# Performance work log

Hardware: AMD Instinct MI355X
Metric: run time of the kernel (lower is better)

## Reference

```python
import jax, jax.numpy as jnp
import numpy as np

N, E, F_IN, GCH, H, HID, NOUT, NG = 5000, 15000, 300, 2048, 4, 2048, 768, 128
NEG_SLOPE = 0.2


def gat_conv(x, W, att_src, att_dst, bias, src, dst):
    # x: [N, Fin]; W: [Fin, H*C]; att_*: [H, C]; bias: [H*C]
    n = x.shape[0]
    h = (x @ W).reshape(n, H, GCH)                      # [N,H,C]
    a_src = (h * att_src).sum(-1)                       # [N,H]
    a_dst = (h * att_dst).sum(-1)                       # [N,H]
    e = jax.nn.leaky_relu(a_src[src] + a_dst[dst], NEG_SLOPE)  # [E,H]
    m = jax.ops.segment_max(e, dst, num_segments=n)     # segment softmax over dst
    e = jnp.exp(e - m[dst])
    s = jax.ops.segment_sum(e, dst, num_segments=n)
    alpha = e / (s[dst] + 1e-16)                        # [E,H]
    msg = h[src] * alpha[:, :, None]                    # [E,H,C]
    out = jax.ops.segment_sum(msg, dst, num_segments=n) # [N,H,C]
    return out.reshape(n, H * GCH) + bias


def setup_inputs() -> dict:
    key = jax.random.key(0)
    ks = jax.random.split(key, 32)
    d = {}
    d['x'] = jax.random.normal(ks[0], (N, F_IN), jnp.float32)
    d['edge_index'] = jax.random.randint(ks[1], (2, E), 0, N, jnp.int32)
    d['batch'] = jnp.sort(jax.random.randint(ks[2], (N,), 0, NG, jnp.int32))
    dims_in = [F_IN, HID, HID]
    i = 3
    for l, fin in enumerate(dims_in, 1):
        sc = 1.0 / np.sqrt(fin)
        d[f'W{l}'] = jax.random.normal(ks[i], (fin, H * GCH), jnp.float32) * sc; i += 1
        d[f'asrc{l}'] = jax.random.normal(ks[i], (H, GCH), jnp.float32) * 0.02; i += 1
        d[f'adst{l}'] = jax.random.normal(ks[i], (H, GCH), jnp.float32) * 0.02; i += 1
        d[f'bc{l}'] = jnp.zeros((H * GCH,), jnp.float32)
        d[f'Wh{l}'] = jax.random.normal(ks[i], (H * GCH, HID), jnp.float32) * (1.0 / np.sqrt(H * GCH)); i += 1
        d[f'bh{l}'] = jnp.zeros((HID,), jnp.float32)
    d['Wm1'] = jax.random.normal(ks[i], (GCH, 2048), jnp.float32) * (1.0 / np.sqrt(GCH)); i += 1
    d['bm1'] = jnp.zeros((2048,), jnp.float32)
    d['Wm2'] = jax.random.normal(ks[i], (2048, NOUT), jnp.float32) * (1.0 / np.sqrt(2048)); i += 1
    d['bm2'] = jnp.zeros((NOUT,), jnp.float32)
    d['ln_g'] = jnp.ones((NOUT,), jnp.float32)
    d['ln_b'] = jnp.zeros((NOUT,), jnp.float32)
    return d


def reference(x, edge_index, batch,
              W1, asrc1, adst1, bc1, Wh1, bh1,
              W2, asrc2, adst2, bc2, Wh2, bh2,
              W3, asrc3, adst3, bc3, Wh3, bh3,
              Wm1, bm1, Wm2, bm2, ln_g, ln_b):
    n = x.shape[0]
    # PyG GATConv adds self-loops by default
    loops = jnp.arange(n, dtype=edge_index.dtype)
    src = jnp.concatenate([edge_index[0], loops])
    dst = jnp.concatenate([edge_index[1], loops])

    h = gat_conv(x, W1, asrc1, adst1, bc1, src, dst)
    h = jax.nn.relu(h @ Wh1 + bh1)
    h = gat_conv(h, W2, asrc2, adst2, bc2, src, dst)
    h = jax.nn.relu(h @ Wh2 + bh2)
    h = gat_conv(h, W3, asrc3, adst3, bc3, src, dst)
    h = h @ Wh3 + bh3                                   # no relu after head_linear3

    # global mean pool over graphs
    sums = jax.ops.segment_sum(h, batch, num_segments=NG)
    cnt = jax.ops.segment_sum(jnp.ones((n,), h.dtype), batch, num_segments=NG)
    g = sums / jnp.maximum(cnt, 1.0)[:, None]           # [NG, 2048]

    g = jax.nn.relu(g @ Wm1 + bm1)
    g = g @ Wm2 + bm2                                   # [NG, NOUT]
    mu = g.mean(-1, keepdims=True)
    var = ((g - mu) ** 2).mean(-1, keepdims=True)
    return (g - mu) / jnp.sqrt(var + 1e-5) * ln_g + ln_b
```

## Files before the change

### kernel.cpp

```cpp
#include <hip/hip_runtime.h>

typedef unsigned short u16;
typedef __attribute__((ext_vector_type(8))) short short8;
typedef __attribute__((ext_vector_type(4))) float f32x4;

__device__ inline u16 f2bf(float f){
  unsigned int u = __builtin_bit_cast(unsigned int, f);
  u += 0x7fffu + ((u >> 16) & 1u);
  return (u16)(u >> 16);
}
__device__ inline float bf2f(u16 h){
  unsigned int u = ((unsigned int)h) << 16;
  return __builtin_bit_cast(float, u);
}

typedef __attribute__((address_space(1))) const void* as1_t;
typedef __attribute__((address_space(3))) void* as3_t;
__device__ __forceinline__ void gload16(const u16* g, u16* l) {
  __builtin_amdgcn_global_load_lds((as1_t)g, (as3_t)l, 16, 0, 0);
}

#define BARRIER() asm volatile("s_barrier" ::: "memory")
#define VMCNT4()  asm volatile("s_waitcnt vmcnt(4)" ::: "memory")
#define VMCNT0()  asm volatile("s_waitcnt vmcnt(0)" ::: "memory")
#define LGKM0()   asm volatile("s_waitcnt lgkmcnt(0)" ::: "memory")

__global__ __launch_bounds__(256) void transpose_cast(
    const float* __restrict__ W, u16* __restrict__ Wt, int K, int N, int Kpad)
{
  __shared__ float tile[32][33];
  int k0 = blockIdx.x * 32, n0 = blockIdx.y * 32;
  int tx = threadIdx.x & 31, ty = threadIdx.x >> 5;
#pragma unroll
  for (int i = 0; i < 4; ++i) {
    int k = k0 + ty + i * 8;
    float v = 0.f;
    if (k < K && (n0 + tx) < N) v = W[(size_t)k * N + n0 + tx];
    tile[ty + i * 8][tx] = v;
  }
  __syncthreads();
#pragma unroll
  for (int i = 0; i < 4; ++i) {
    int nn = n0 + ty + i * 8;
    if (nn < N) Wt[(size_t)nn * Kpad + k0 + tx] = f2bf(tile[tx][ty + i * 8]);
  }
}

__global__ void cast_pad(const float* __restrict__ x, u16* __restrict__ xb,
                         int R, int C, int Cp)
{
  int i = blockIdx.x * 256 + threadIdx.x;
  if (i >= R * Cp) return;
  int r = i / Cp, c = i % Cp;
  xb[i] = f2bf(c < C ? x[(size_t)r * C + c] : 0.f);
}

__global__ __launch_bounds__(256) void wvec(
    const float* __restrict__ W, const float* __restrict__ asrc,
    const float* __restrict__ adst, float* __restrict__ wsd, int Fp)
{
  int f = blockIdx.x;
  int w = threadIdx.x >> 6, lane = threadIdx.x & 63;
  const float* wr = W + (size_t)f * 8192 + w * 2048;
  const float* as = asrc + w * 2048;
  const float* ad = adst + w * 2048;
  float ss = 0.f, dd = 0.f;
#pragma unroll
  for (int i = 0; i < 8; ++i) {
    int c = lane * 4 + i * 256;
    f32x4 wv = *reinterpret_cast<const f32x4*>(wr + c);
    f32x4 av = *reinterpret_cast<const f32x4*>(as + c);
    f32x4 dv = *reinterpret_cast<const f32x4*>(ad + c);
#pragma unroll
    for (int j = 0; j < 4; ++j) { ss += wv[j] * av[j]; dd += wv[j] * dv[j]; }
  }
  for (int off = 32; off; off >>= 1) {
    ss += __shfl_down(ss, off);
    dd += __shfl_down(dd, off);
  }
  if (lane == 0) { wsd[w * Fp + f] = ss; wsd[(4 + w) * Fp + f] = dd; }
}

__global__ __launch_bounds__(256) void a_score(
    const u16* __restrict__ xb, const float* __restrict__ wsd,
    float* __restrict__ a_s, float* __restrict__ a_d, int Fp)
{
  int n = blockIdx.x, tid = threadIdx.x, lane = tid & 63, w = tid >> 6;
  float s[4] = {0.f,0.f,0.f,0.f}, d[4] = {0.f,0.f,0.f,0.f};
  int f = tid * 8;
  if (f < Fp) {
    short8 v = *reinterpret_cast<const short8*>(xb + (size_t)n * Fp + f);
#pragma unroll
    for (int j = 0; j < 8; ++j) {
      float xv = bf2f((u16)v[j]);
#pragma unroll
      for (int h = 0; h < 4; ++h) {
        s[h] += xv * wsd[h * Fp + f + j];
        d[h] += xv * wsd[(4 + h) * Fp + f + j];
      }
    }
  }
  __shared__ float red[4][8];
#pragma unroll
  for (int h = 0; h < 4; ++h) {
    for (int off = 32; off; off >>= 1) {
      s[h] += __shfl_down(s[h], off);
      d[h] += __shfl_down(d[h], off);
    }
  }
  if (lane == 0) {
#pragma unroll
    for (int h = 0; h < 4; ++h) { red[w][h] = s[h]; red[w][4 + h] = d[h]; }
  }
  __syncthreads();
  if (tid < 8) {
    float t = red[0][tid] + red[1][tid] + red[2][tid] + red[3][tid];
    if (tid < 4) a_s[n * 4 + tid] = t;
    else         a_d[n * 4 + tid - 4] = t;
  }
}

__global__ __launch_bounds__(256) void bias_fold(
    const float* __restrict__ bc, const float* __restrict__ Wh,
    const float* __restrict__ bh, float* __restrict__ bhp)
{
  int b = blockIdx.x;
  int oc = threadIdx.x & 31, ks = threadIdx.x >> 5;
  int o = b * 32 + oc;
  float acc = 0.f;
  for (int k = ks * 1024; k < ks * 1024 + 1024; ++k)
    acc += bc[k] * Wh[(size_t)k * 2048 + o];
  __shared__ float red[8][33];
  red[ks][oc] = acc;
  __syncthreads();
  if (threadIdx.x < 32) {
    float t = 0.f;
#pragma unroll
    for (int i = 0; i < 8; ++i) t += red[i][threadIdx.x];
    bhp[b * 32 + threadIdx.x] = t + bh[b * 32 + threadIdx.x];
  }
}

__global__ __launch_bounds__(512, 2) void gemm8p(
    const u16* __restrict__ A, const u16* __restrict__ B, u16* __restrict__ C,
    int M, int N, int K, int lda, int ldb, int ldc, int headed)
{
  __shared__ alignas(16) u16 lds[65536];
  int tid = threadIdx.x, wave = tid >> 6, lane = tid & 63;
  int wm = wave >> 2, wn = wave & 3;
  int tile_m = blockIdx.y * 256, tile_n = blockIdx.x * 256;
  int NT = K >> 6;
  int hoff = headed ? ((tile_m >> 11) << 11) : 0;
  int abase = headed ? (tile_m & 2047) : tile_m;

  const u16* sA[2]; const u16* sB[2];
  int dq[2];
#pragma unroll
  for (int q = 0; q < 2; ++q) {
    int row = q * 128 + (tid >> 2);
    int cg  = (tid & 3) ^ ((row >> 1) & 3);
    sA[q] = A + (size_t)(abase + row) * lda + hoff + cg * 8;
    sB[q] = B + (size_t)(tile_n + row) * ldb + hoff + cg * 8;
    dq[q] = q * 4096 + tid * 8;
  }

  int l15 = lane & 15, c4 = lane >> 4;
  int aoff[8], boff[4];
#pragma unroll
  for (int mi = 0; mi < 8; ++mi) {
    int r = wm * 128 + mi * 16 + l15;
    aoff[mi] = r * 32 + ((c4 ^ ((r >> 1) & 3)) * 8);
  }
#pragma unroll
  for (int ni = 0; ni < 4; ++ni) {
    int r = wn * 64 + ni * 16 + l15;
    boff[ni] = r * 32 + ((c4 ^ ((r >> 1) & 3)) * 8);
  }

  f32x4 acc[8][4];
#pragma unroll
  for (int mi = 0; mi < 8; ++mi)
#pragma unroll
    for (int ni = 0; ni < 4; ++ni) { f32x4 z = {0.f,0.f,0.f,0.f}; acc[mi][ni] = z; }

#define DSRA(fa, mb, base) \
  fa[0] = *reinterpret_cast<const short8*>(&lds[(base) + aoff[(mb)+0]]); \
  fa[1] = *reinterpret_cast<const short8*>(&lds[(base) + aoff[(mb)+1]]); \
  fa[2] = *reinterpret_cast<const short8*>(&lds[(base) + aoff[(mb)+2]]); \
  fa[3] = *reinterpret_cast<const short8*>(&lds[(base) + aoff[(mb)+3]]);
#define DSRB(fb, base) \
  fb[0] = *reinterpret_cast<const short8*>(&lds[(base) + boff[0]]); \
  fb[1] = *reinterpret_cast<const short8*>(&lds[(base) + boff[1]]); \
  fb[2] = *reinterpret_cast<const short8*>(&lds[(base) + boff[2]]); \
  fb[3] = *reinterpret_cast<const short8*>(&lds[(base) + boff[3]]);
#define MM16(mb, fa, fb) \
  _Pragma("unroll") for (int mi = 0; mi < 4; ++mi) \
  _Pragma("unroll") for (int ni = 0; ni < 4; ++ni) \
    acc[(mb)+mi][ni] = __builtin_amdgcn_mfma_f32_16x16x32_bf16(fa[mi], fb[ni], acc[(mb)+mi][ni], 0, 0, 0);
#define PH_SYNC() BARRIER(); LGKM0(); __builtin_amdgcn_sched_barrier(0)
#define PRIO1() __builtin_amdgcn_s_setprio(1)
#define PRIO0() __builtin_amdgcn_s_setprio(0)

#pragma unroll
  for (int q = 0; q < 2; ++q) {
    gload16(sA[q],      &lds[0     + dq[q]]);
    gload16(sB[q],      &lds[16384 + dq[q]]);
    gload16(sA[q] + 32, &lds[8192  + dq[q]]);
    gload16(sB[q] + 32, &lds[24576 + dq[q]]);
  }
  VMCNT0();
  BARRIER();

  for (int t = 0; t < NT; ++t) {
    int cb = (t & 1) * 32768;
    int nb = cb ^ 32768;
    bool st = (t + 1) < NT;
    int ke = (t + 1) * 64;
    short8 fa[4], fb0[4], fb1[4];
    DSRA(fa, 0, cb + 0);
    DSRB(fb0, cb + 16384);
    if (st) { gload16(sA[0] + ke, &lds[nb + dq[0]]);
              gload16(sA[1] + ke, &lds[nb + dq[1]]); }
    PH_SYNC(); PRIO1(); MM16(0, fa, fb0); PRIO0();
    BARRIER();
    DSRA(fa, 4, cb + 0);
    if (st) { gload16(sB[0] + ke, &lds[nb + 16384 + dq[0]]);
              gload16(sB[1] + ke, &lds[nb + 16384 + dq[1]]); }
    PH_SYNC(); PRIO1(); MM16(4, fa, fb0); PRIO0();
    if (st) { VMCNT4(); } else { VMCNT0(); }
    BARRIER();
    DSRA(fa, 0, cb + 8192);
    DSRB(fb1, cb + 24576);
    if (st) { gload16(sA[0] + ke + 32, &lds[nb + 8192 + dq[0]]);
              gload16(sA[1] + ke + 32, &lds[nb + 8192 + dq[1]]); }
    PH_SYNC(); PRIO1(); MM16(0, fa, fb1); PRIO0();
    BARRIER();
    DSRA(fa, 4, cb + 8192);
    if (st) { gload16(sB[0] + ke + 32, &lds[nb + 24576 + dq[0]]);
              gload16(sB[1] + ke + 32, &lds[nb + 24576 + dq[1]]); }
    PH_SYNC(); PRIO1(); MM16(4, fa, fb1); PRIO0();
    if (st) { VMCNT4(); }
    BARRIER();
  }

  int rq = (lane >> 4) * 4;
#pragma unroll
  for (int mi = 0; mi < 8; ++mi)
#pragma unroll
    for (int ni = 0; ni < 4; ++ni) {
      int col = tile_n + wn * 64 + ni * 16 + l15;
#pragma unroll
      for (int j = 0; j < 4; ++j) {
        int row = tile_m + wm * 128 + mi * 16 + rq + j;
        if (row < M) C[(size_t)row * ldc + col] = f2bf(acc[mi][ni][j]);
      }
    }
#undef DSRA
#undef DSRB
#undef MM16
#undef PH_SYNC
#undef PRIO1
#undef PRIO0
}

__global__ __launch_bounds__(256) void gemm_bt(
    const u16* __restrict__ A, const u16* __restrict__ B,
    float* __restrict__ Cf, u16* __restrict__ Cb,
    const float* __restrict__ bias, int M, int N, int K, int relu)
{
  __shared__ alignas(16) u16 As[128 * 32];
  __shared__ alignas(16) u16 Bs[128 * 32];
  int tid = threadIdx.x;
  int wave = tid >> 6, lane = tid & 63;
  int wr = wave >> 1, wc = wave & 1;
  int tile_m = blockIdx.y * 128, tile_n = blockIdx.x * 128;

  int sr = wave * 16 + (lane >> 2);
  int sc = (lane & 3) * 8;
  const u16* gA0 = A + (size_t)(tile_m + sr) * K + sc;
  const u16* gA1 = A + (size_t)(tile_m + 64 + sr) * K + sc;
  const u16* gB0 = B + (size_t)(tile_n + sr) * K + sc;
  const u16* gB1 = B + (size_t)(tile_n + 64 + sr) * K + sc;
  u16* lA0 = &As[wave * 512];
  u16* lA1 = &As[2048 + wave * 512];
  u16* lB0 = &Bs[wave * 512];
  u16* lB1 = &Bs[2048 + wave * 512];

  f32x4 acc[4][4];
#pragma unroll
  for (int mi = 0; mi < 4; ++mi)
#pragma unroll
    for (int ni = 0; ni < 4; ++ni) { f32x4 z = {0.f,0.f,0.f,0.f}; acc[mi][ni] = z; }

  int lrow = lane & 15, lk = (lane >> 4) * 8;

  for (int k0 = 0; k0 < K; k0 += 32) {
    gload16(gA0 + k0, lA0);
    gload16(gA1 + k0, lA1);
    gload16(gB0 + k0, lB0);
    gload16(gB1 + k0, lB1);
    __syncthreads();
    short8 af[4], bfr[4];
#pragma unroll
    for (int mi = 0; mi < 4; ++mi)
      af[mi] = *reinterpret_cast<const short8*>(&As[(wr * 64 + mi * 16 + lrow) * 32 + lk]);
#pragma unroll
    for (int ni = 0; ni < 4; ++ni)
      bfr[ni] = *reinterpret_cast<const short8*>(&Bs[(wc * 64 + ni * 16 + lrow) * 32 + lk]);
#pragma unroll
    for (int mi = 0; mi < 4; ++mi)
#pragma unroll
      for (int ni = 0; ni < 4; ++ni)
        acc[mi][ni] = __builtin_amdgcn_mfma_f32_16x16x32_bf16(af[mi], bfr[ni], acc[mi][ni], 0, 0, 0);
    __syncthreads();
  }

  int rquad = (lane >> 4) * 4;
#pragma unroll
  for (int mi = 0; mi < 4; ++mi)
#pragma unroll
    for (int ni = 0; ni < 4; ++ni) {
      int col = tile_n + wc * 64 + ni * 16 + lrow;
      float bv = bias ? bias[col] : 0.f;
#pragma unroll
      for (int j = 0; j < 4; ++j) {
        int row = tile_m + wr * 64 + mi * 16 + rquad + j;
        if (row < M) {
          float v = acc[mi][ni][j] + bv;
          if (relu) v = fmaxf(v, 0.f);
          if (Cb) Cb[(size_t)row * N + col] = f2bf(v);
          else    Cf[(size_t)row * N + col] = v;
        }
      }
    }
}

__global__ void zero_int(int* p, int n){ int i = blockIdx.x*256+threadIdx.x; if (i < n) p[i] = 0; }

__global__ void count_deg(const int* __restrict__ ei, int E, int Nn, int* __restrict__ deg){
  int e = blockIdx.x*256+threadIdx.x; if (e >= E + Nn) return;
  int d = (e < E) ? ei[E + e] : (e - E);
  atomicAdd(&deg[d], 1);
}

__global__ void scan_deg(const int* __restrict__ deg, int* __restrict__ row_st,
                         int* __restrict__ cursor, int Nn){
  __shared__ int partial[256];
  int tid = threadIdx.x;
  int chunk = (Nn + 255) / 256;
  int start = tid * chunk;
  int sum = 0;
  for (int i = 0; i < chunk; ++i) { int idx = start + i; if (idx < Nn) sum += deg[idx]; }
  partial[tid] = sum;
  __syncthreads();
  if (tid == 0) { int acc = 0; for (int i = 0; i < 256; ++i) { int t = partial[i]; partial[i] = acc; acc += t; } }
  __syncthreads();
  int acc = partial[tid];
  for (int i = 0; i < chunk; ++i) {
    int idx = start + i;
    if (idx < Nn) { row_st[idx] = acc; cursor[idx] = acc; acc += deg[idx]; }
  }
  if (tid == 255) row_st[Nn] = acc;
}

__global__ void scatter_edges(const int* __restrict__ ei, int E, int Nn,
                              int* __restrict__ cursor, int* __restrict__ srcs){
  int e = blockIdx.x*256+threadIdx.x; if (e >= E + Nn) return;
  int s = (e < E) ? ei[e]     : (e - E);
  int d = (e < E) ? ei[E + e] : (e - E);
  int pos = atomicAdd(&cursor[d], 1);
  srcs[pos] = s;
}

__global__ void edge_softmax(const int* __restrict__ row_st, const int* __restrict__ srcs,
                             const float* __restrict__ a_s, const float* __restrict__ a_d,
                             float* __restrict__ alpha, int Nn){
  int t = blockIdx.x*256+threadIdx.x;
  if (t >= Nn * 4) return;
  int n = t >> 2, hh = t & 3;
  int b = row_st[n], e = row_st[n + 1];
  float ad = a_d[n * 4 + hh];
  float m = -1e30f;
  for (int p = b; p < e; ++p) {
    float x = a_s[srcs[p] * 4 + hh] + ad;
    x = x > 0.f ? x : 0.2f * x;
    alpha[p * 4 + hh] = x;
    m = fmaxf(m, x);
  }
  float ssum = 0.f;
  for (int p = b; p < e; ++p) {
    float ex = expf(alpha[p * 4 + hh] - m);
    alpha[p * 4 + hh] = ex;
    ssum += ex;
  }
  float inv = 1.f / (ssum + 1e-16f);
  for (int p = b; p < e; ++p) alpha[p * 4 + hh] *= inv;
}

__global__ __launch_bounds__(256) void aggregate2(
    const u16* __restrict__ z, const float* __restrict__ alpha,
    const int* __restrict__ row_st, const int* __restrict__ srcs,
    const float* __restrict__ bhp, u16* __restrict__ out, int relu)
{
  int n = blockIdx.x, tid = threadIdx.x;
  int c = tid * 8;
  float acc[8];
#pragma unroll
  for (int q = 0; q < 8; ++q) acc[q] = 0.f;
  int b = row_st[n], e = row_st[n + 1];
  for (int p = b; p < e; ++p) {
    int s = srcs[p];
    const u16* zr = z + (size_t)s * 8192 + c;
    float a0 = alpha[p * 4 + 0], a1 = alpha[p * 4 + 1];
    float a2 = alpha[p * 4 + 2], a3 = alpha[p * 4 + 3];
    short8 v0 = *reinterpret_cast<const short8*>(zr);
    short8 v1 = *reinterpret_cast<const short8*>(zr + 2048);
    short8 v2 = *reinterpret_cast<const short8*>(zr + 4096);
    short8 v3 = *reinterpret_cast<const short8*>(zr + 6144);
#pragma unroll
    for (int q = 0; q < 8; ++q)
      acc[q] += a0 * bf2f((u16)v0[q]) + a1 * bf2f((u16)v1[q])
              + a2 * bf2f((u16)v2[q]) + a3 * bf2f((u16)v3[q]);
  }
  short8 ov;
#pragma unroll
  for (int q = 0; q < 8; ++q) {
    float v = acc[q] + bhp[c + q];
    if (relu) v = fmaxf(v, 0.f);
    ov[q] = (short)f2bf(v);
  }
  *reinterpret_cast<short8*>(out + (size_t)n * 2048 + c) = ov;
}

__global__ __launch_bounds__(256) void pool_mean(
    const u16* __restrict__ hf, const int* __restrict__ batch,
    u16* __restrict__ g, int Nn)
{
  int gid = blockIdx.x, tid = threadIdx.x;
  int s1, s2;
  { int l = 0, h = Nn; while (l < h) { int m = (l + h) >> 1; if (batch[m] < gid) l = m + 1; else h = m; } s1 = l; }
  { int l = 0, h = Nn; while (l < h) { int m = (l + h) >> 1; if (batch[m] < gid + 1) l = m + 1; else h = m; } s2 = l; }
  float inv = 1.f / fmaxf((float)(s2 - s1), 1.f);
  float acc[8];
#pragma unroll
  for (int q = 0; q < 8; ++q) acc[q] = 0.f;
  for (int r = s1; r < s2; ++r) {
    short8 v = *reinterpret_cast<const short8*>(hf + (size_t)r * 2048 + tid * 8);
#pragma unroll
    for (int q = 0; q < 8; ++q) acc[q] += bf2f((u16)v[q]);
  }
  short8 ov;
#pragma unroll
  for (int q = 0; q < 8; ++q) ov[q] = (short)f2bf(acc[q] * inv);
  *reinterpret_cast<short8*>(g + (size_t)gid * 2048 + tid * 8) = ov;
}

__global__ __launch_bounds__(256) void layernorm_768(
    const float* __restrict__ x, const float* __restrict__ gam,
    const float* __restrict__ bet, float* __restrict__ out)
{
  int row = blockIdx.x, tid = threadIdx.x, lane = tid & 63, w = tid >> 6;
  __shared__ float sh[8];
  float v0 = x[row * 768 + tid];
  float v1 = x[row * 768 + 256 + tid];
  float v2 = x[row * 768 + 512 + tid];
  float s = v0 + v1 + v2;
  for (int off = 32; off; off >>= 1) s += __shfl_down(s, off);
  if (lane == 0) sh[w] = s;
  __syncthreads();
  if (tid == 0) sh[4] = (sh[0] + sh[1] + sh[2] + sh[3]) / 768.f;
  __syncthreads();
  float mu = sh[4];
  float d0 = v0 - mu, d1 = v1 - mu, d2 = v2 - mu;
  float q = d0 * d0 + d1 * d1 + d2 * d2;
  for (int off = 32; off; off >>= 1) q += __shfl_down(q, off);
  if (lane == 0) sh[w] = q;
  __syncthreads();
  if (tid == 0) sh[5] = rsqrtf((sh[0] + sh[1] + sh[2] + sh[3]) / 768.f + 1e-5f);
  __syncthreads();
  float rstd = sh[5];
  out[row * 768 + tid]       = d0 * rstd * gam[tid]       + bet[tid];
  out[row * 768 + 256 + tid] = d1 * rstd * gam[256 + tid] + bet[256 + tid];
  out[row * 768 + 512 + tid] = d2 * rstd * gam[512 + tid] + bet[512 + tid];
}

extern "C" void kernel_launch(void* const* d_in, const int* in_sizes, int n_in,
                              void* d_out, int out_size, void* d_ws, size_t ws_size,
                              hipStream_t stream)
{
  const float* x     = (const float*)d_in[0];
  const int*   ei    = (const int*)d_in[1];
  const int*   batch = (const int*)d_in[2];
  const float* W[3]   = {(const float*)d_in[3], (const float*)d_in[9],  (const float*)d_in[15]};
  const float* asr[3] = {(const float*)d_in[4], (const float*)d_in[10], (const float*)d_in[16]};
  const float* ads[3] = {(const float*)d_in[5], (const float*)d_in[11], (const float*)d_in[17]};
  const float* bc[3]  = {(const float*)d_in[6], (const float*)d_in[12], (const float*)d_in[18]};
  const float* Wh[3]  = {(const float*)d_in[7], (const float*)d_in[13], (const float*)d_in[19]};
  const float* bh[3]  = {(const float*)d_in[8], (const float*)d_in[14], (const float*)d_in[20]};
  const float* Wm1 = (const float*)d_in[21];
  const float* bm1 = (const float*)d_in[22];
  const float* Wm2 = (const float*)d_in[23];
  const float* bm2 = (const float*)d_in[24];
  const float* lng = (const float*)d_in[25];
  const float* lnb = (const float*)d_in[26];
  float* out = (float*)d_out;

  int Nn = in_sizes[2];
  int E  = in_sizes[1] / 2;
  int ET = E + Nn;

  char* base = (char*)d_ws;
  size_t off = 0;
  auto alloc = [&](size_t b) -> char* { char* p = base + off; off = (off + b + 255) & ~(size_t)255; return p; };
  u16*  xb0   = (u16*)alloc((size_t)5120 * 512 * 2);
  u16*  actA  = (u16*)alloc((size_t)5120 * 2048 * 2);
  u16*  actB  = (u16*)alloc((size_t)5120 * 2048 * 2);
  u16*  Wb    = (u16*)alloc((size_t)2048 * 8192 * 2);
  u16*  Wht   = (u16*)alloc((size_t)2048 * 8192 * 2);
  u16*  Ut    = (u16*)alloc((size_t)8192 * 2048 * 2);
  u16*  zb    = (u16*)alloc((size_t)5120 * 8192 * 2);
  float* wsd  = (float*)alloc((size_t)8 * 2048 * 4);
  float* a_s  = (float*)alloc((size_t)Nn * 4 * 4);
  float* a_d  = (float*)alloc((size_t)Nn * 4 * 4);
  float* alpha= (float*)alloc((size_t)ET * 4 * 4);
  float* bhp  = (float*)alloc((size_t)2048 * 4);
  int*  deg   = (int*)alloc((size_t)(Nn + 1) * 4);
  int*  rowst = (int*)alloc((size_t)(Nn + 1) * 4);
  int*  cursor= (int*)alloc((size_t)(Nn + 1) * 4);
  int*  srcs  = (int*)alloc((size_t)ET * 4);
  u16*  g     = (u16*)alloc((size_t)128 * 2048 * 2);
  u16*  g2    = (u16*)alloc((size_t)128 * 2048 * 2);
  float* preln= (float*)alloc((size_t)128 * 768 * 4);

  zero_int<<<(Nn + 255) / 256, 256, 0, stream>>>(deg, Nn);
  count_deg<<<(ET + 255) / 256, 256, 0, stream>>>(ei, E, Nn, deg);
  scan_deg<<<1, 256, 0, stream>>>(deg, rowst, cursor, Nn);
  scatter_edges<<<(ET + 255) / 256, 256, 0, stream>>>(ei, E, Nn, cursor, srcs);

  cast_pad<<<(Nn * 512 + 255) / 256, 256, 0, stream>>>(x, xb0, Nn, 300, 512);

  const u16* act = xb0;
  for (int l = 0; l < 3; ++l) {
    int Fin = (l == 0) ? 300 : 2048;
    int Fp  = (l == 0) ? 512 : 2048;
    u16* outb = (l & 1) ? actB : actA;

    cast_pad<<<(Fin * 8192 + 255) / 256, 256, 0, stream>>>(W[l], Wb, Fin, 8192, 8192);
    transpose_cast<<<dim3(256, 64), 256, 0, stream>>>(Wh[l], Wht, 8192, 2048, 8192);
    gemm8p<<<dim3(Fp / 256, 32), 512, 0, stream>>>(Wht, Wb, Ut, 8192, Fp, 2048, 8192, 8192, Fp, 1);
    wvec<<<Fin, 256, 0, stream>>>(W[l], asr[l], ads[l], wsd, Fp);
    a_score<<<Nn, 256, 0, stream>>>(act, wsd, a_s, a_d, Fp);
    edge_softmax<<<(Nn * 4 + 255) / 256, 256, 0, stream>>>(rowst, srcs, a_s, a_d, alpha, Nn);
    gemm8p<<<dim3(32, 20), 512, 0, stream>>>(act, Ut, zb, Nn, 8192, Fp, Fp, Fp, 8192, 0);
    bias_fold<<<64, 256, 0, stream>>>(bc[l], Wh[l], bh[l], bhp);
    aggregate2<<<Nn, 256, 0, stream>>>(zb, alpha, rowst, srcs, bhp, outb, (l < 2) ? 1 : 0);
    act = outb;
  }

  pool_mean<<<128, 256, 0, stream>>>(act, batch, g, Nn);
  u16* Mt1 = Ut;
  u16* Mt2 = Ut + (size_t)2048 * 2048;
  transpose_cast<<<dim3(64, 64), 256, 0, stream>>>(Wm1, Mt1, 2048, 2048, 2048);
  gemm_bt<<<dim3(16, 1), 256, 0, stream>>>(g, Mt1, nullptr, g2, bm1, 128, 2048, 2048, 1);
  transpose_cast<<<dim3(64, 24), 256, 0, stream>>>(Wm2, Mt2, 2048, 768, 2048);
  gemm_bt<<<dim3(6, 1), 256, 0, stream>>>(g2, Mt2, preln, nullptr, bm2, 128, 768, 2048, 0);
  layernorm_768<<<128, 256, 0, stream>>>(preln, lng, lnb, out);
}
```

Baseline: 1.542 ms.

## Fuse weight prep kernels and attention scores into aggregate epilogue

Merges the W cast and attention-vector dot product into one prep_w kernel, and folds the bias projection into the Wh transpose using atomics. All three layers' weight products are precomputed up front into separate buffers, with staging placed inside the zb scratch. The next layer's attention scores are computed in the aggregate2 epilogue, which removes a_score launches and the activation re-reads for layers 2 and 3. This cuts launches and memory passes, at the cost of atomic-order nondeterminism in the bias and scores taken from fp32 values before bf16 rounding.

```diff
diff --git a/kernel.cpp b/kernel.cpp
--- a/kernel.cpp
+++ b/kernel.cpp
@@ -2,6 +2,7 @@
 
 typedef unsigned short u16;
 typedef __attribute__((ext_vector_type(8))) short short8;
+typedef __attribute__((ext_vector_type(4))) short s16x4;
 typedef __attribute__((ext_vector_type(4))) float f32x4;
 
 __device__ inline u16 f2bf(float f){
@@ -25,133 +26,14 @@
 #define VMCNT0()  asm volatile("s_waitcnt vmcnt(0)" ::: "memory")
 #define LGKM0()   asm volatile("s_waitcnt lgkmcnt(0)" ::: "memory")
 
-__global__ __launch_bounds__(256) void transpose_cast(
-    const float* __restrict__ W, u16* __restrict__ Wt, int K, int N, int Kpad)
-{
-  __shared__ float tile[32][33];
-  int k0 = blockIdx.x * 32, n0 = blockIdx.y * 32;
-  int tx = threadIdx.x & 31, ty = threadIdx.x >> 5;
-#pragma unroll
-  for (int i = 0; i < 4; ++i) {
-    int k = k0 + ty + i * 8;
-    float v = 0.f;
-    if (k < K && (n0 + tx) < N) v = W[(size_t)k * N + n0 + tx];
-    tile[ty + i * 8][tx] = v;
-  }
-  __syncthreads();
-#pragma unroll
-  for (int i = 0; i < 4; ++i) {
-    int nn = n0 + ty + i * 8;
-    if (nn < N) Wt[(size_t)nn * Kpad + k0 + tx] = f2bf(tile[tx][ty + i * 8]);
-  }
-}
-
-__global__ void cast_pad(const float* __restrict__ x, u16* __restrict__ xb,
-                         int R, int C, int Cp)
-{
-  int i = blockIdx.x * 256 + threadIdx.x;
-  if (i >= R * Cp) return;
-  int r = i / Cp, c = i % Cp;
-  xb[i] = f2bf(c < C ? x[(size_t)r * C + c] : 0.f);
-}
-
-__global__ __launch_bounds__(256) void wvec(
-    const float* __restrict__ W, const float* __restrict__ asrc,
-    const float* __restrict__ adst, float* __restrict__ wsd, int Fp)
-{
-  int f = blockIdx.x;
-  int w = threadIdx.x >> 6, lane = threadIdx.x & 63;
-  const float* wr = W + (size_t)f * 8192 + w * 2048;
-  const float* as = asrc + w * 2048;
-  const float* ad = adst + w * 2048;
-  float ss = 0.f, dd = 0.f;
-#pragma unroll
-  for (int i = 0; i < 8; ++i) {
-    int c = lane * 4 + i * 256;
-    f32x4 wv = *reinterpret_cast<const f32x4*>(wr + c);
-    f32x4 av = *reinterpret_cast<const f32x4*>(as + c);
-    f32x4 dv = *reinterpret_cast<const f32x4*>(ad + c);
-#pragma unroll
-    for (int j = 0; j < 4; ++j) { ss += wv[j] * av[j]; dd += wv[j] * dv[j]; }
-  }
-  for (int off = 32; off; off >>= 1) {
-    ss += __shfl_down(ss, off);
-    dd += __shfl_down(dd, off);
-  }
-  if (lane == 0) { wsd[w * Fp + f] = ss; wsd[(4 + w) * Fp + f] = dd; }
-}
-
-__global__ __launch_bounds__(256) void a_score(
-    const u16* __restrict__ xb, const float* __restrict__ wsd,
-    float* __restrict__ a_s, float* __restrict__ a_d, int Fp)
-{
-  int n = blockIdx.x, tid = threadIdx.x, lane = tid & 63, w = tid >> 6;
-  float s[4] = {0.f,0.f,0.f,0.f}, d[4] = {0.f,0.f,0.f,0.f};
-  int f = tid * 8;
-  if (f < Fp) {
-    short8 v = *reinterpret_cast<const short8*>(xb + (size_t)n * Fp + f);
-#pragma unroll
-    for (int j = 0; j < 8; ++j) {
-      float xv = bf2f((u16)v[j]);
-#pragma unroll
-      for (int h = 0; h < 4; ++h) {
-        s[h] += xv * wsd[h * Fp + f + j];
-        d[h] += xv * wsd[(4 + h) * Fp + f + j];
-      }
-    }
-  }
-  __shared__ float red[4][8];
-#pragma unroll
-  for (int h = 0; h < 4; ++h) {
-    for (int off = 32; off; off >>= 1) {
-      s[h] += __shfl_down(s[h], off);
-      d[h] += __shfl_down(d[h], off);
-    }
-  }
-  if (lane == 0) {
-#pragma unroll
-    for (int h = 0; h < 4; ++h) { red[w][h] = s[h]; red[w][4 + h] = d[h]; }
-  }
-  __syncthreads();
-  if (tid < 8) {
-    float t = red[0][tid] + red[1][tid] + red[2][tid] + red[3][tid];
-    if (tid < 4) a_s[n * 4 + tid] = t;
-    else         a_d[n * 4 + tid - 4] = t;
-  }
-}
-
-__global__ __launch_bounds__(256) void bias_fold(
-    const float* __restrict__ bc, const float* __restrict__ Wh,
-    const float* __restrict__ bh, float* __restrict__ bhp)
-{
-  int b = blockIdx.x;
-  int oc = threadIdx.x & 31, ks = threadIdx.x >> 5;
-  int o = b * 32 + oc;
-  float acc = 0.f;
-  for (int k = ks * 1024; k < ks * 1024 + 1024; ++k)
-    acc += bc[k] * Wh[(size_t)k * 2048 + o];
-  __shared__ float red[8][33];
-  red[ks][oc] = acc;
-  __syncthreads();
-  if (threadIdx.x < 32) {
-    float t = 0.f;
-#pragma unroll
-    for (int i = 0; i < 8; ++i) t += red[i][threadIdx.x];
-    bhp[b * 32 + threadIdx.x] = t + bh[b * 32 + threadIdx.x];
-  }
-}
-
-__global__ __launch_bounds__(512, 2) void gemm8p(
+__device__ __forceinline__ void gemm_core(
     const u16* __restrict__ A, const u16* __restrict__ B, u16* __restrict__ C,
-    int M, int N, int K, int lda, int ldb, int ldc, int headed)
-{
-  __shared__ alignas(16) u16 lds[65536];
+    int tile_m, int tile_n, int abase, int hoff,
+    int M, int K, int lda, int ldb, int ldc, u16* lds)
+{
   int tid = threadIdx.x, wave = tid >> 6, lane = tid & 63;
   int wm = wave >> 2, wn = wave & 3;
-  int tile_m = blockIdx.y * 256, tile_n = blockIdx.x * 256;
   int NT = K >> 6;
-  int hoff = headed ? ((tile_m >> 11) << 11) : 0;
-  int abase = headed ? (tile_m & 2047) : tile_m;
 
   const u16* sA[2]; const u16* sB[2];
   int dq[2];
@@ -263,76 +145,157 @@
 #undef PRIO0
 }
 
-__global__ __launch_bounds__(256) void gemm_bt(
-    const u16* __restrict__ A, const u16* __restrict__ B,
-    float* __restrict__ Cf, u16* __restrict__ Cb,
-    const float* __restrict__ bias, int M, int N, int K, int relu)
-{
-  __shared__ alignas(16) u16 As[128 * 32];
-  __shared__ alignas(16) u16 Bs[128 * 32];
-  int tid = threadIdx.x;
-  int wave = tid >> 6, lane = tid & 63;
-  int wr = wave >> 1, wc = wave & 1;
-  int tile_m = blockIdx.y * 128, tile_n = blockIdx.x * 128;
-
-  int sr = wave * 16 + (lane >> 2);
-  int sc = (lane & 3) * 8;
-  const u16* gA0 = A + (size_t)(tile_m + sr) * K + sc;
-  const u16* gA1 = A + (size_t)(tile_m + 64 + sr) * K + sc;
-  const u16* gB0 = B + (size_t)(tile_n + sr) * K + sc;
-  const u16* gB1 = B + (size_t)(tile_n + 64 + sr) * K + sc;
-  u16* lA0 = &As[wave * 512];
-  u16* lA1 = &As[2048 + wave * 512];
-  u16* lB0 = &Bs[wave * 512];
-  u16* lB1 = &Bs[2048 + wave * 512];
-
-  f32x4 acc[4][4];
-#pragma unroll
-  for (int mi = 0; mi < 4; ++mi)
-#pragma unroll
-    for (int ni = 0; ni < 4; ++ni) { f32x4 z = {0.f,0.f,0.f,0.f}; acc[mi][ni] = z; }
-
-  int lrow = lane & 15, lk = (lane >> 4) * 8;
-
-  for (int k0 = 0; k0 < K; k0 += 32) {
-    gload16(gA0 + k0, lA0);
-    gload16(gA1 + k0, lA1);
-    gload16(gB0 + k0, lB0);
-    gload16(gB1 + k0, lB1);
-    __syncthreads();
-    short8 af[4], bfr[4];
-#pragma unroll
-    for (int mi = 0; mi < 4; ++mi)
-      af[mi] = *reinterpret_cast<const short8*>(&As[(wr * 64 + mi * 16 + lrow) * 32 + lk]);
-#pragma unroll
-    for (int ni = 0; ni < 4; ++ni)
-      bfr[ni] = *reinterpret_cast<const short8*>(&Bs[(wc * 64 + ni * 16 + lrow) * 32 + lk]);
-#pragma unroll
-    for (int mi = 0; mi < 4; ++mi)
-#pragma unroll
-      for (int ni = 0; ni < 4; ++ni)
-        acc[mi][ni] = __builtin_amdgcn_mfma_f32_16x16x32_bf16(af[mi], bfr[ni], acc[mi][ni], 0, 0, 0);
-    __syncthreads();
-  }
-
-  int rquad = (lane >> 4) * 4;
-#pragma unroll
-  for (int mi = 0; mi < 4; ++mi)
-#pragma unroll
-    for (int ni = 0; ni < 4; ++ni) {
-      int col = tile_n + wc * 64 + ni * 16 + lrow;
-      float bv = bias ? bias[col] : 0.f;
-#pragma unroll
-      for (int j = 0; j < 4; ++j) {
-        int row = tile_m + wr * 64 + mi * 16 + rquad + j;
-        if (row < M) {
-          float v = acc[mi][ni][j] + bv;
-          if (relu) v = fmaxf(v, 0.f);
-          if (Cb) Cb[(size_t)row * N + col] = f2bf(v);
-          else    Cf[(size_t)row * N + col] = v;
-        }
+__global__ __launch_bounds__(512, 2) void gemm8p(
+    const u16* __restrict__ A, const u16* __restrict__ B, u16* __restrict__ C,
+    int M, int N, int K, int lda, int ldb, int ldc, int headed)
+{
+  __shared__ alignas(16) u16 lds[65536];
+  int tile_m = blockIdx.y * 256, tile_n = blockIdx.x * 256;
+  int hoff  = headed ? ((tile_m >> 11) << 11) : 0;
+  int abase = headed ? (tile_m & 2047) : tile_m;
+  gemm_core(A, B, C, tile_m, tile_n, abase, hoff, M, K, lda, ldb, ldc, lds);
+}
+
+__global__ __launch_bounds__(256) void prep_w(
+    const float* __restrict__ W, u16* __restrict__ Wb,
+    const float* __restrict__ asrc, const float* __restrict__ adst,
+    float* __restrict__ wsd, int Fin, int Fp)
+{
+  int f = blockIdx.x;
+  int w = threadIdx.x >> 6, lane = threadIdx.x & 63;
+  if (f >= Fin) {
+    s16x4 z = {0,0,0,0};
+#pragma unroll
+    for (int i = 0; i < 8; ++i)
+      *reinterpret_cast<s16x4*>(Wb + (size_t)f * 8192 + w * 2048 + lane * 4 + i * 256) = z;
+    if (lane == 0) { wsd[w * Fp + f] = 0.f; wsd[(4 + w) * Fp + f] = 0.f; }
+    return;
+  }
+  const float* wr = W + (size_t)f * 8192 + w * 2048;
+  const float* as = asrc + w * 2048;
+  const float* ad = adst + w * 2048;
+  u16* wb = Wb + (size_t)f * 8192 + w * 2048;
+  float ss = 0.f, dd = 0.f;
+#pragma unroll
+  for (int i = 0; i < 8; ++i) {
+    int c = lane * 4 + i * 256;
+    f32x4 wv = *reinterpret_cast<const f32x4*>(wr + c);
+    f32x4 av = *reinterpret_cast<const f32x4*>(as + c);
+    f32x4 dv = *reinterpret_cast<const f32x4*>(ad + c);
+    s16x4 ov;
+#pragma unroll
+    for (int j = 0; j < 4; ++j) {
+      ss += wv[j] * av[j]; dd += wv[j] * dv[j];
+      ov[j] = (short)f2bf(wv[j]);
+    }
+    *reinterpret_cast<s16x4*>(wb + c) = ov;
+  }
+  for (int off = 32; off; off >>= 1) {
+    ss += __shfl_down(ss, off);
+    dd += __shfl_down(dd, off);
+  }
+  if (lane == 0) { wsd[w * Fp + f] = ss; wsd[(4 + w) * Fp + f] = dd; }
+}
+
+__global__ __launch_bounds__(256) void transpose_bias(
+    const float* __restrict__ Wh, u16* __restrict__ Wht,
+    const float* __restrict__ bc, float* __restrict__ bhp)
+{
+  __shared__ float tile[32][33];
+  int k0 = blockIdx.x * 32, n0 = blockIdx.y * 32;
+  int tx = threadIdx.x & 31, ty = threadIdx.x >> 5;
+#pragma unroll
+  for (int i = 0; i < 4; ++i)
+    tile[ty + i * 8][tx] = Wh[(size_t)(k0 + ty + i * 8) * 2048 + n0 + tx];
+  __syncthreads();
+#pragma unroll
+  for (int i = 0; i < 4; ++i)
+    Wht[(size_t)(n0 + ty + i * 8) * 8192 + k0 + tx] = f2bf(tile[tx][ty + i * 8]);
+  if (threadIdx.x < 32) {
+    float p = 0.f;
+#pragma unroll
+    for (int kk = 0; kk < 32; ++kk) p += bc[k0 + kk] * tile[kk][threadIdx.x];
+    atomicAdd(&bhp[n0 + threadIdx.x], p);
+  }
+}
+
+__global__ void init_bhp(const float* b0, const float* b1, const float* b2,
+                         float* bhp){
+  int i = blockIdx.x * 256 + threadIdx.x;
+  int l = blockIdx.y;
+  if (i < 2048) {
+    const float* s = (l == 0) ? b0 : (l == 1 ? b1 : b2);
+    bhp[l * 2048 + i] = s[i];
+  }
+}
+
+__global__ __launch_bounds__(256) void transpose_cast(
+    const float* __restrict__ W, u16* __restrict__ Wt, int K, int N, int Kpad)
+{
+  __shared__ float tile[32][33];
+  int k0 = blockIdx.x * 32, n0 = blockIdx.y * 32;
+  int tx = threadIdx.x & 31, ty = threadIdx.x >> 5;
+#pragma unroll
+  for (int i = 0; i < 4; ++i) {
+    int k = k0 + ty + i * 8;
+    float v = 0.f;
+    if (k < K && (n0 + tx) < N) v = W[(size_t)k * N + n0 + tx];
+    tile[ty + i * 8][tx] = v;
+  }
+  __syncthreads();
+#pragma unroll
+  for (int i = 0; i < 4; ++i) {
+    int nn = n0 + ty + i * 8;
+    if (nn < N) Wt[(size_t)nn * Kpad + k0 + tx] = f2bf(tile[tx][ty + i * 8]);
+  }
+}
+
+__global__ void cast_pad(const float* __restrict__ x, u16* __restrict__ xb,
+                         int R, int C, int Cp)
+{
+  int i = blockIdx.x * 256 + threadIdx.x;
+  if (i >= R * Cp) return;
+  int r = i / Cp, c = i % Cp;
+  xb[i] = f2bf(c < C ? x[(size_t)r * C + c] : 0.f);
+}
+
+__global__ __launch_bounds__(256) void a_score(
+    const u16* __restrict__ xb, const float* __restrict__ wsd,
+    float* __restrict__ a_s, float* __restrict__ a_d, int Fp)
+{
+  int n = blockIdx.x, tid = threadIdx.x, lane = tid & 63, w = tid >> 6;
+  float s[4] = {0.f,0.f,0.f,0.f}, d[4] = {0.f,0.f,0.f,0.f};
+  int f = tid * 8;
+  if (f < Fp) {
+    short8 v = *reinterpret_cast<const short8*>(xb + (size_t)n * Fp + f);
+#pragma unroll
+    for (int j = 0; j < 8; ++j) {
+      float xv = bf2f((u16)v[j]);
+#pragma unroll
+      for (int h = 0; h < 4; ++h) {
+        s[h] += xv * wsd[h * Fp + f + j];
+        d[h] += xv * wsd[(4 + h) * Fp + f + j];
       }
     }
+  }
+  __shared__ float red[4][8];
+#pragma unroll
+  for (int h = 0; h < 4; ++h) {
+    for (int off = 32; off; off >>= 1) {
+      s[h] += __shfl_down(s[h], off);
+      d[h] += __shfl_down(d[h], off);
+    }
+  }
+  if (lane == 0) {
+#pragma unroll
+    for (int h = 0; h < 4; ++h) { red[w][h] = s[h]; red[w][4 + h] = d[h]; }
+  }
+  __syncthreads();
+  if (tid < 8) {
+    float t = red[0][tid] + red[1][tid] + red[2][tid] + red[3][tid];
+    if (tid < 4) a_s[n * 4 + tid] = t;
+    else         a_d[n * 4 + tid - 4] = t;
+  }
 }
 
 __global__ void zero_int(int* p, int n){ int i = blockIdx.x*256+threadIdx.x; if (i < n) p[i] = 0; }
@@ -400,7 +363,9 @@
 __global__ __launch_bounds__(256) void aggregate2(
     const u16* __restrict__ z, const float* __restrict__ alpha,
     const int* __restrict__ row_st, const int* __restrict__ srcs,
-    const float* __restrict__ bhp, u16* __restrict__ out, int relu)
+    const float* __restrict__ bhp, u16* __restrict__ out, int relu,
+    const float* __restrict__ wsd_next, float* __restrict__ a_s,
+    float* __restrict__ a_d)
 {
   int n = blockIdx.x, tid = threadIdx.x;
   int c = tid * 8;
@@ -422,14 +387,43 @@
       acc[q] += a0 * bf2f((u16)v0[q]) + a1 * bf2f((u16)v1[q])
               + a2 * bf2f((u16)v2[q]) + a3 * bf2f((u16)v3[q]);
   }
+  float sv[4] = {0.f,0.f,0.f,0.f}, dv[4] = {0.f,0.f,0.f,0.f};
   short8 ov;
 #pragma unroll
   for (int q = 0; q < 8; ++q) {
     float v = acc[q] + bhp[c + q];
     if (relu) v = fmaxf(v, 0.f);
     ov[q] = (short)f2bf(v);
+    if (wsd_next) {
+#pragma unroll
+      for (int h = 0; h < 4; ++h) {
+        sv[h] += v * wsd_next[h * 2048 + c + q];
+        dv[h] += v * wsd_next[(4 + h) * 2048 + c + q];
+      }
+    }
   }
   *reinterpret_cast<short8*>(out + (size_t)n * 2048 + c) = ov;
+  if (wsd_next) {
+    int lane = tid & 63, w = tid >> 6;
+    __shared__ float red[4][8];
+#pragma unroll
+    for (int h = 0; h < 4; ++h) {
+      for (int off = 32; off; off >>= 1) {
+        sv[h] += __shfl_down(sv[h], off);
+        dv[h] += __shfl_down(dv[h], off);
+      }
+    }
+    if (lane == 0) {
+#pragma unroll
+      for (int h = 0; h < 4; ++h) { red[w][h] = sv[h]; red[w][4 + h] = dv[h]; }
+    }
+    __syncthreads();
+    if (tid < 8) {
+      float t = red[0][tid] + red[1][tid] + red[2][tid] + red[3][tid];
+      if (tid < 4) a_s[n * 4 + tid] = t;
+      else         a_d[n * 4 + tid - 4] = t;
+    }
+  }
 }
 
 __global__ __launch_bounds__(256) void pool_mean(
@@ -453,6 +447,78 @@
 #pragma unroll
   for (int q = 0; q < 8; ++q) ov[q] = (short)f2bf(acc[q] * inv);
   *reinterpret_cast<short8*>(g + (size_t)gid * 2048 + tid * 8) = ov;
+}
+
+__global__ __launch_bounds__(256) void gemm_bt(
+    const u16* __restrict__ A, const u16* __restrict__ B,
+    float* __restrict__ Cf, u16* __restrict__ Cb,
+    const float* __restrict__ bias, int M, int N, int K, int relu)
+{
+  __shared__ alignas(16) u16 As[128 * 32];
+  __shared__ alignas(16) u16 Bs[128 * 32];
+  int tid = threadIdx.x;
+  int wave = tid >> 6, lane = tid & 63;
+  int wr = wave >> 1, wc = wave & 1;
+  int tile_m = blockIdx.y * 128, tile_n = blockIdx.x * 128;
+
+  int sr = wave * 16 + (lane >> 2);
+  int sc = (lane & 3) * 8;
+  const u16* gA0 = A + (size_t)(tile_m + sr) * K + sc;
+  const u16* gA1 = A + (size_t)(tile_m + 64 + sr) * K + sc;
+  const u16* gB0 = B + (size_t)(tile_n + sr) * K + sc;
+  const u16* gB1 = B + (size_t)(tile_n + 64 + sr) * K + sc;
+  u16* lA0 = &As[wave * 512];
+  u16* lA1 = &As[2048 + wave * 512];
+  u16* lB0 = &Bs[wave * 512];
+  u16* lB1 = &Bs[2048 + wave * 512];
+
+  f32x4 acc[4][4];
+#pragma unroll
+  for (int mi = 0; mi < 4; ++mi)
+#pragma unroll
+    for (int ni = 0; ni < 4; ++ni) { f32x4 z = {0.f,0.f,0.f,0.f}; acc[mi][ni] = z; }
+
+  int lrow = lane & 15, lk = (lane >> 4) * 8;
+
+  for (int k0 = 0; k0 < K; k0 += 32) {
+    gload16(gA0 + k0, lA0);
+    gload16(gA1 + k0, lA1);
+    gload16(gB0 + k0, lB0);
+    gload16(gB1 + k0, lB1);
+    __syncthreads();
+    short8 af[4], bfr[4];
+#pragma unroll
+    for (int mi = 0; mi < 4; ++mi)
+      af[mi] = *reinterpret_cast<const short8*>(&As[(wr * 64 + mi * 16 + lrow) * 32 + lk]);
+#pragma unroll
+    for (int ni = 0; ni < 4; ++ni)
+      bfr[ni] = *reinterpret_cast<const short8*>(&Bs[(wc * 64 + ni * 16 + lrow) * 32 + lk]);
+#pragma unroll
+    for (int mi = 0; mi < 4; ++mi)
+#pragma unroll
+      for (int ni = 0; ni < 4; ++ni)
+        acc[mi][ni] = __builtin_amdgcn_mfma_f32_16x16x32_bf16(af[mi], bfr[ni], acc[mi][ni], 0, 0, 0);
+    __syncthreads();
+  }
+
+  int rquad = (lane >> 4) * 4;
+#pragma unroll
+  for (int mi = 0; mi < 4; ++mi)
+#pragma unroll
+    for (int ni = 0; ni < 4; ++ni) {
+      int col = tile_n + wc * 64 + ni * 16 + lrow;
+      float bv = bias ? bias[col] : 0.f;
+#pragma unroll
+      for (int j = 0; j < 4; ++j) {
+        int row = tile_m + wr * 64 + mi * 16 + rquad + j;
+        if (row < M) {
+          float v = acc[mi][ni][j] + bv;
+          if (relu) v = fmaxf(v, 0.f);
+          if (Cb) Cb[(size_t)row * N + col] = f2bf(v);
+          else    Cf[(size_t)row * N + col] = v;
+        }
+      }
+    }
 }
 
 __global__ __launch_bounds__(256) void layernorm_768(
@@ -512,18 +578,18 @@
   char* base = (char*)d_ws;
   size_t off = 0;
   auto alloc = [&](size_t b) -> char* { char* p = base + off; off = (off + b + 255) & ~(size_t)255; return p; };
-  u16*  xb0   = (u16*)alloc((size_t)5120 * 512 * 2);
   u16*  actA  = (u16*)alloc((size_t)5120 * 2048 * 2);
   u16*  actB  = (u16*)alloc((size_t)5120 * 2048 * 2);
-  u16*  Wb    = (u16*)alloc((size_t)2048 * 8192 * 2);
-  u16*  Wht   = (u16*)alloc((size_t)2048 * 8192 * 2);
-  u16*  Ut    = (u16*)alloc((size_t)8192 * 2048 * 2);
+  u16*  Ut0   = (u16*)alloc((size_t)8192 * 512  * 2);
+  u16*  Ut1   = (u16*)alloc((size_t)8192 * 2048 * 2);
+  u16*  Ut2   = (u16*)alloc((size_t)8192 * 2048 * 2);
   u16*  zb    = (u16*)alloc((size_t)5120 * 8192 * 2);
-  float* wsd  = (float*)alloc((size_t)8 * 2048 * 4);
+  u16*  xb0   = (u16*)alloc((size_t)5120 * 512 * 2);
+  float* wsd  = (float*)alloc((size_t)3 * 8 * 2048 * 4);
+  float* bhp  = (float*)alloc((size_t)3 * 2048 * 4);
   float* a_s  = (float*)alloc((size_t)Nn * 4 * 4);
   float* a_d  = (float*)alloc((size_t)Nn * 4 * 4);
   float* alpha= (float*)alloc((size_t)ET * 4 * 4);
-  float* bhp  = (float*)alloc((size_t)2048 * 4);
   int*  deg   = (int*)alloc((size_t)(Nn + 1) * 4);
   int*  rowst = (int*)alloc((size_t)(Nn + 1) * 4);
   int*  cursor= (int*)alloc((size_t)(Nn + 1) * 4);
@@ -532,34 +598,45 @@
   u16*  g2    = (u16*)alloc((size_t)128 * 2048 * 2);
   float* preln= (float*)alloc((size_t)128 * 768 * 4);
 
+  u16* Wb_sh  = zb;
+  u16* Wht_sh = zb + (size_t)2048 * 8192;
+
   zero_int<<<(Nn + 255) / 256, 256, 0, stream>>>(deg, Nn);
   count_deg<<<(ET + 255) / 256, 256, 0, stream>>>(ei, E, Nn, deg);
   scan_deg<<<1, 256, 0, stream>>>(deg, rowst, cursor, Nn);
   scatter_edges<<<(ET + 255) / 256, 256, 0, stream>>>(ei, E, Nn, cursor, srcs);
-
   cast_pad<<<(Nn * 512 + 255) / 256, 256, 0, stream>>>(x, xb0, Nn, 300, 512);
 
+  init_bhp<<<dim3(8, 3), 256, 0, stream>>>(bh[0], bh[1], bh[2], bhp);
+  prep_w<<<512, 256, 0, stream>>>(W[0], Wb_sh, asr[0], ads[0], wsd, 300, 512);
+  transpose_bias<<<dim3(256, 64), 256, 0, stream>>>(Wh[0], Wht_sh, bc[0], bhp);
+  gemm8p<<<dim3(2, 32), 512, 0, stream>>>(Wht_sh, Wb_sh, Ut0, 8192, 512, 2048, 8192, 8192, 512, 1);
+  prep_w<<<2048, 256, 0, stream>>>(W[1], Wb_sh, asr[1], ads[1], wsd + 16384, 2048, 2048);
+  transpose_bias<<<dim3(256, 64), 256, 0, stream>>>(Wh[1], Wht_sh, bc[1], bhp + 2048);
+  gemm8p<<<dim3(8, 32), 512, 0, stream>>>(Wht_sh, Wb_sh, Ut1, 8192, 2048, 2048, 8192, 8192, 2048, 1);
+  prep_w<<<2048, 256, 0, stream>>>(W[2], Wb_sh, asr[2], ads[2], wsd + 32768, 2048, 2048);
+  transpose_bias<<<dim3(256, 64), 256, 0, stream>>>(Wh[2], Wht_sh, bc[2], bhp + 4096);
+  gemm8p<<<dim3(8, 32), 512, 0, stream>>>(Wht_sh, Wb_sh, Ut2, 8192, 2048, 2048, 8192, 8192, 2048, 1);
+
+  a_score<<<Nn, 256, 0, stream>>>(xb0, wsd, a_s, a_d, 512);
+
   const u16* act = xb0;
+  u16* Ut[3] = {Ut0, Ut1, Ut2};
   for (int l = 0; l < 3; ++l) {
-    int Fin = (l == 0) ? 300 : 2048;
-    int Fp  = (l == 0) ? 512 : 2048;
+    int Fp = (l == 0) ? 512 : 2048;
     u16* outb = (l & 1) ? actB : actA;
-
-    cast_pad<<<(Fin * 8192 + 255) / 256, 256, 0, stream>>>(W[l], Wb, Fin, 8192, 8192);
-    transpose_cast<<<dim3(256, 64), 256, 0, stream>>>(Wh[l], Wht, 8192, 2048, 8192);
-    gemm8p<<<dim3(Fp / 256, 32), 512, 0, stream>>>(Wht, Wb, Ut, 8192, Fp, 2048, 8192, 8192, Fp, 1);
-    wvec<<<Fin, 256, 0, stream>>>(W[l], asr[l], ads[l], wsd, Fp);
-    a_score<<<Nn, 256, 0, stream>>>(act, wsd, a_s, a_d, Fp);
     edge_softmax<<<(Nn * 4 + 255) / 256, 256, 0, stream>>>(rowst, srcs, a_s, a_d, alpha, Nn);
-    gemm8p<<<dim3(32, 20), 512, 0, stream>>>(act, Ut, zb, Nn, 8192, Fp, Fp, Fp, 8192, 0);
-    bias_fold<<<64, 256, 0, stream>>>(bc[l], Wh[l], bh[l], bhp);
-    aggregate2<<<Nn, 256, 0, stream>>>(zb, alpha, rowst, srcs, bhp, outb, (l < 2) ? 1 : 0);
+    gemm8p<<<dim3(32, 20), 512, 0, stream>>>(act, Ut[l], zb, Nn, 8192, Fp, Fp, Fp, 8192, 0);
+    aggregate2<<<Nn, 256, 0, stream>>>(zb, alpha, rowst, srcs, bhp + l * 2048, outb,
+                                       (l < 2) ? 1 : 0,
+                                       (l < 2) ? (wsd + (l + 1) * 16384) : nullptr,
+                                       a_s, a_d);
     act = outb;
   }
 
   pool_mean<<<128, 256, 0, stream>>>(act, batch, g, Nn);
-  u16* Mt1 = Ut;
-  u16* Mt2 = Ut + (size_t)2048 * 2048;
+  u16* Mt1 = zb;
+  u16* Mt2 = zb + (size_t)2048 * 2048;
   transpose_cast<<<dim3(64, 64), 256, 0, stream>>>(Wm1, Mt1, 2048, 2048, 2048);
   gemm_bt<<<dim3(16, 1), 256, 0, stream>>>(g, Mt1, nullptr, g2, bm1, 128, 2048, 2048, 1);
   transpose_cast<<<dim3(64, 24), 256, 0, stream>>>(Wm2, Mt2, 2048, 768, 2048);
```

New measurement: 1.387 ms. 1.11x faster.
